# Kernel optimization log

Measured on AMD Instinct MI355X. Metric: run time of the kernel, lower is better.

The kernel has to match this reference:

```python
import jax, jax.numpy as jnp
import numpy as np

B, T, S = 16, 128, 128          # batch, temporal, spatial (road segments)
NIN, SIN = 3, 1                 # number / speed input feature sizes
NH, SH, DH = 64, 64, 128        # number-enc / speed-enc / decoder hidden
T_PREDICT = 20


def _p(k, shape, scale=0.05):
    return (jax.random.normal(k, shape) * scale).astype(jnp.float32)


def setup_inputs() -> dict:
    key = jax.random.key(0)
    ks = jax.random.split(key, 16)
    inp = {"input_data": jax.random.normal(ks[0], (B, T, S, NIN + SIN), dtype=jnp.float32)}
    # seg_model cells: LSTM gates driven by input x, own hidden h, spatial neighbors h_after/h_before
    inp.update(
        n_Wx=_p(ks[1], (NIN, 4 * NH)), n_Wh=_p(ks[2], (NH, 4 * NH)),
        n_Wa=_p(ks[3], (NH, 4 * NH)), n_Wb=_p(ks[4], (NH, 4 * NH)),
        n_b=jnp.zeros((4 * NH,), jnp.float32),
        s_Wx=_p(ks[5], (SIN, 4 * SH)), s_Wh=_p(ks[6], (SH, 4 * SH)),
        s_Wa=_p(ks[7], (SH, 4 * SH)), s_Wb=_p(ks[8], (SH, 4 * SH)),
        s_b=jnp.zeros((4 * SH,), jnp.float32),
        d_Wx=_p(ks[9], (NH + SH, 4 * DH)), d_Wh=_p(ks[10], (DH, 4 * DH)),
        d_Wa=_p(ks[11], (DH, 4 * DH)), d_Wb=_p(ks[12], (DH, 4 * DH)),
        d_b=jnp.zeros((4 * DH,), jnp.float32),
        on_W=_p(ks[13], (DH, 1)), on_b=jnp.zeros((1,), jnp.float32),
        os_W=_p(ks[14], (DH, 1)), os_b=jnp.zeros((1,), jnp.float32),
    )
    return inp


def _cell(x, h, c, ha, hb, Wx, Wh, Wa, Wb, b):
    g = x @ Wx + h @ Wh + ha @ Wa + hb @ Wb + b
    i, f, u, o = jnp.split(g, 4, axis=-1)
    c2 = jax.nn.sigmoid(f) * c + jax.nn.sigmoid(i) * jnp.tanh(u)
    return jax.nn.sigmoid(o) * jnp.tanh(c2), c2


def _shift(h):
    # h_after[s] = h[s+1], h_before[s] = h[s-1], zero-padded at the boundary
    z = jnp.zeros_like(h[:, :1])
    return jnp.concatenate([h[:, 1:], z], axis=1), jnp.concatenate([z, h[:, :-1]], axis=1)


def _next_input(former_number, next_x, output):
    # output: [B,S,2] = (number_out, speed_out)
    speed_in = next_x[:, :1, 3:]                                    # [B,1,1]
    speed_next = jnp.concatenate([speed_in, output[:, 1:, 1:]], axis=1)
    inflow = jnp.concatenate([next_x[:, 0:1, 1:2], output[:, :-1, 0:1]], axis=1)
    number_calc = former_number[:, :, 2:3] + inflow - output[:, :, 0:1]
    return jnp.concatenate([output[:, :, 0:1], inflow, number_calc, speed_next], axis=2)


def reference(input_data, n_Wx, n_Wh, n_Wa, n_Wb, n_b,
              s_Wx, s_Wh, s_Wa, s_Wb, s_b,
              d_Wx, d_Wh, d_Wa, d_Wb, d_b,
              on_W, on_b, os_W, os_b):
    b, t, s, _ = input_data.shape
    zeros = lambda hdim: jnp.zeros((b, s, hdim), input_data.dtype)
    init = (zeros(NH), zeros(NH), zeros(SH), zeros(SH), zeros(DH), zeros(DH))

    def step(carry, xs):
        hn, cn, hs, cs, hd, cd = carry
        x_t, x_tp1 = xs
        hn_a, hn_b = _shift(hn)
        hs_a, hs_b = _shift(hs)
        hd_a, hd_b = _shift(hd)
        num = x_t[:, :, :NIN]
        spd = x_t[:, :, NIN:]
        hn, cn = _cell(num, hn, cn, hn_a, hn_b, n_Wx, n_Wh, n_Wa, n_Wb, n_b)
        hs, cs = _cell(spd, hs, cs, hs_a, hs_b, s_Wx, s_Wh, s_Wa, s_Wb, s_b)
        dec_in = jnp.concatenate([hn, hs], axis=2)
        hd, cd = _cell(dec_in, hd, cd, hd_a, hd_b, d_Wx, d_Wh, d_Wa, d_Wb, d_b)
        output = jnp.concatenate([hd @ on_W + on_b, hd @ os_W + os_b], axis=2)
        data = _next_input(num, x_tp1, output)
        return (hn, cn, hs, cs, hd, cd), data

    xs = (jnp.moveaxis(input_data[:, :-1], 1, 0),   # x_t,   t = 0..T-2 (time-major)
          jnp.moveaxis(input_data[:, 1:], 1, 0))    # x_{t+1}
    _, datas = jax.lax.scan(step, init, xs)          # [T-1, B, S, 4]
    # original writes outputs only for time >= t_predict; slicing is equivalent
    return jnp.moveaxis(datas[T_PREDICT:], 0, 1)     # [B, T-T_PREDICT-1, S, 4]
```

## Files before the change

### kernel.cpp

```cpp
#include <hip/hip_runtime.h>

constexpr int B_ = 16, T_ = 128, S_ = 128;
constexpr int ROWS = B_ * S_;
constexpr int NSTEPS = T_ - 1;
constexpr int TPRED = 20;
constexpr int TOUT = NSTEPS - TPRED;
constexpr int TB = 512;
constexpr int NBLK = 256;

constexpr int OFF_HN = 0;
constexpr int OFF_HS = OFF_HN + 131072;
constexpr int OFF_HD = OFF_HS + 131072;
constexpr int OFF_CN = OFF_HD + 262144;
constexpr int OFF_CS = OFF_CN + 131072;
constexpr int OFF_CD = OFF_CS + 131072;
constexpr int OFF_OUTS = OFF_CD + 262144;
constexpr int ZERO_DW = OFF_OUTS + NSTEPS * ROWS * 2;
constexpr int OFF_NPK = ZERO_DW;
constexpr int NPK_DW = 16 * 7 * 256;
constexpr int OFF_SPK = OFF_NPK + NPK_DW;
constexpr int OFF_DPK = OFF_SPK + NPK_DW;
constexpr int DPK_DW = 32 * 16 * 256;
constexpr int PACK_DWORDS = 2 * NPK_DW + DPK_DW;

typedef _Float16 half8 __attribute__((ext_vector_type(8)));
typedef float float4v __attribute__((ext_vector_type(4)));

__device__ __forceinline__ float sigm(float x) { return 1.f / (1.f + __expf(-x)); }
__device__ __forceinline__ float tanh_(float x) { return 2.f / (1.f + __expf(-2.f * x)) - 1.f; }
__device__ __forceinline__ unsigned int pack2(float a, float b) {
    union { unsigned int u; _Float16 h[2]; } x;
    x.h[0] = (_Float16)a; x.h[1] = (_Float16)b; return x.u;
}

__global__ __launch_bounds__(256) void pack_weights(
    const float* __restrict__ nWx, const float* __restrict__ nWh,
    const float* __restrict__ nWa, const float* __restrict__ nWb, const float* __restrict__ nb,
    const float* __restrict__ sWx, const float* __restrict__ sWh,
    const float* __restrict__ sWa, const float* __restrict__ sWb, const float* __restrict__ sb,
    const float* __restrict__ dWx, const float* __restrict__ dWh,
    const float* __restrict__ dWa, const float* __restrict__ dWb,
    unsigned int* __restrict__ wsu)
{
    int idx = blockIdx.x * 256 + threadIdx.x;
    if (idx >= PACK_DWORDS) return;
    if (idx < 2 * NPK_DW) {
        bool isS = idx >= NPK_DW;
        int dn = isS ? idx - NPK_DW : idx;
        int tile = dn >> 8;
        int e = (dn & 255) * 2;
        int lane = e >> 3, j0 = e & 7;
        int quad = lane >> 4;
        int nt = tile / 7, tt = tile % 7;
        int col = nt * 16 + (lane & 15);
        float v0, v1;
        if (tt < 6) {
            const float* W = isS ? ((tt < 2) ? sWh : (tt < 4) ? sWa : sWb)
                                 : ((tt < 2) ? nWh : (tt < 4) ? nWa : nWb);
            int k = (tt & 1) * 32 + quad * 8 + j0;
            v0 = W[k * 256 + col]; v1 = W[(k + 1) * 256 + col];
        } else {
            int kl = quad * 8 + j0;
            auto xv = [&](int k) -> float {
                if (!isS) { if (k < 3) return nWx[k * 256 + col]; if (k == 3) return nb[col]; return 0.f; }
                else      { if (k == 4) return sWx[col]; if (k == 5) return sb[col]; return 0.f; }
            };
            v0 = xv(kl); v1 = xv(kl + 1);
        }
        wsu[(isS ? OFF_SPK : OFF_NPK) + dn] = pack2(v0, v1);
    } else {
        int dd = idx - 2 * NPK_DW;
        int tile = dd >> 8;
        int e = (dd & 255) * 2;
        int lane = e >> 3, j0 = e & 7;
        int quad = lane >> 4;
        int nt = tile >> 4, tt = tile & 15;
        const float* W = (tt < 4) ? dWx : (tt < 8) ? dWh : (tt < 12) ? dWa : dWb;
        int k = (tt & 3) * 32 + quad * 8 + j0;
        int col = nt * 16 + (lane & 15);
        wsu[OFF_DPK + dd] = pack2(W[k * 512 + col], W[(k + 1) * 512 + col]);
    }
}

__global__ __launch_bounds__(TB) void pipe_kernel(
    int li,
    const float* __restrict__ input,
    const float* __restrict__ db,
    const float* __restrict__ onW, const float* __restrict__ osW,
    float* __restrict__ ws)
{
    const int tid = threadIdx.x;
    const int wave = tid >> 6, lane = tid & 63;
    const int quad = lane >> 4, l15 = lane & 15;
    const int blk = blockIdx.x;

    _Float16* hnG = (_Float16*)((unsigned int*)ws + OFF_HN);
    _Float16* hsG = (_Float16*)((unsigned int*)ws + OFF_HS);
    _Float16* hdG = (_Float16*)((unsigned int*)ws + OFF_HD);
    float* outs = ws + OFF_OUTS;
    const _Float16* pd = (const _Float16*)((const unsigned int*)ws + OFF_DPK);

    __shared__ __align__(16) _Float16 sh_h[34 * 72];
    __shared__ __align__(16) _Float16 sh_xa[32 * 40];
    __shared__ __align__(16) _Float16 sh_hd[34 * 136];
    __shared__ __align__(16) _Float16 sh_dec[32 * 136];
    __shared__ float sh_hdnew[32 * 64];

    if (blk < 128) {
        if (li > 126) return;
        const int pr = blk >> 1, cell = blk & 1;
        const int r0 = pr * 32;
        const int b = r0 >> 7;
        const int s0 = r0 & 127;
        const bool leftOK = (pr & 3) != 0;
        const bool rightOK = (pr & 3) != 3;
        const int pin = (li + 1) & 1, pout = li & 1;
        const _Float16* hC = (cell ? hsG : hnG) + (size_t)pin * ROWS * 64;
        _Float16* hN = (cell ? hsG : hnG) + (size_t)pout * ROWS * 64;
        float* cB = ws + (cell ? OFF_CS : OFF_CN);

        for (int i = tid; i < 1088; i += TB) {
            int row = i >> 5, p = i & 31;
            int grow = r0 + row - 1;
            bool v = (row == 0) ? leftOK : ((row == 33) ? rightOK : true);
            unsigned int val = v ? ((const unsigned int*)hC)[(size_t)grow * 32 + p] : 0u;
            *(unsigned int*)(sh_h + row * 72 + 2 * p) = val;
        }
        for (int i = tid; i < 544; i += TB) {
            int r = i / 17, d = 3 + (i % 17);
            ((unsigned int*)sh_xa)[r * 20 + d] = 0u;
        }
        if (tid < 32) {
            const float* xp = input + ((size_t)(b * T_ + li) * S_ + (s0 + tid)) * 4;
            unsigned int* row = (unsigned int*)sh_xa + tid * 20;
            row[0] = pack2(xp[0], xp[1]);
            row[1] = pack2(xp[2], 1.f);
            row[2] = pack2(xp[3], 1.f);
        }
        __syncthreads();

        const int tl = wave >> 2, sub = wave & 3;
        const _Float16* pk = (const _Float16*)((const unsigned int*)ws + (cell ? OFF_SPK : OFF_NPK));
        const int rb = 1 + tl * 16 + l15;
        half8 ah0 = *(const half8*)(sh_h + rb * 72 + quad * 8);
        half8 ah1 = *(const half8*)(sh_h + rb * 72 + 32 + quad * 8);
        half8 aa0 = *(const half8*)(sh_h + (rb + 1) * 72 + quad * 8);
        half8 aa1 = *(const half8*)(sh_h + (rb + 1) * 72 + 32 + quad * 8);
        half8 ab0 = *(const half8*)(sh_h + (rb - 1) * 72 + quad * 8);
        half8 ab1 = *(const half8*)(sh_h + (rb - 1) * 72 + 32 + quad * 8);
        half8 ax  = *(const half8*)(sh_xa + (tl * 16 + l15) * 40 + quad * 8);
        float4v acc[4];
#pragma unroll
        for (int g = 0; g < 4; ++g) acc[g] = (float4v){0.f, 0.f, 0.f, 0.f};
#pragma unroll
        for (int g = 0; g < 4; ++g) {
            const _Float16* base = pk + (size_t)(4 * g + sub) * 7 * 512 + lane * 8;
            acc[g] = __builtin_amdgcn_mfma_f32_16x16x32_f16(ah0, *(const half8*)(base),        acc[g], 0, 0, 0);
            acc[g] = __builtin_amdgcn_mfma_f32_16x16x32_f16(ah1, *(const half8*)(base + 512),  acc[g], 0, 0, 0);
            acc[g] = __builtin_amdgcn_mfma_f32_16x16x32_f16(aa0, *(const half8*)(base + 1024), acc[g], 0, 0, 0);
            acc[g] = __builtin_amdgcn_mfma_f32_16x16x32_f16(aa1, *(const half8*)(base + 1536), acc[g], 0, 0, 0);
            acc[g] = __builtin_amdgcn_mfma_f32_16x16x32_f16(ab0, *(const half8*)(base + 2048), acc[g], 0, 0, 0);
            acc[g] = __builtin_amdgcn_mfma_f32_16x16x32_f16(ab1, *(const half8*)(base + 2560), acc[g], 0, 0, 0);
            acc[g] = __builtin_amdgcn_mfma_f32_16x16x32_f16(ax,  *(const half8*)(base + 3072), acc[g], 0, 0, 0);
        }
        size_t cIdx = ((size_t)((pr * 2 + tl) * 4 + sub) * 64 + lane) * 4;
        float4v cold = *(const float4v*)(cB + cIdx);
        float4v cnew;
        const int kcol = 16 * sub + l15;
#pragma unroll
        for (int r = 0; r < 4; ++r) {
            float c2 = sigm(acc[1][r]) * cold[r] + sigm(acc[0][r]) * tanh_(acc[2][r]);
            float h2 = sigm(acc[3][r]) * tanh_(c2);
            cnew[r] = c2;
            int row = tl * 16 + quad * 4 + r;
            hN[(size_t)(r0 + row) * 64 + kcol] = (_Float16)h2;
        }
        *(float4v*)(cB + cIdx) = cnew;
    } else {
        if (li < 1) return;
        const int bb = blk - 128;
        const int pr = bb >> 1, ch = bb & 1;
        const int t = li - 1;
        const int r0 = pr * 32;
        const bool leftOK = (pr & 3) != 0;
        const bool rightOK = (pr & 3) != 3;
        const int pinD = li & 1;
        const int poutD = (li - 1) & 1;
        const int pdec = (li - 1) & 1;
        const _Float16* hdC = hdG + (size_t)pinD * ROWS * 128;
        _Float16* hdN = hdG + (size_t)poutD * ROWS * 128;
        const _Float16* hnC = hnG + (size_t)pdec * ROWS * 64;
        const _Float16* hsC = hsG + (size_t)pdec * ROWS * 64;
        float* cd = ws + OFF_CD;

        for (int i = tid; i < 2176; i += TB) {
            int row = i >> 6, p = i & 63;
            int grow = r0 + row - 1;
            bool v = (row == 0) ? leftOK : ((row == 33) ? rightOK : true);
            unsigned int val = v ? ((const unsigned int*)hdC)[(size_t)grow * 64 + p] : 0u;
            *(unsigned int*)(sh_hd + row * 136 + 2 * p) = val;
        }
        for (int i = tid; i < 2048; i += TB) {
            bool isHs = i >= 1024;
            int j = isHs ? i - 1024 : i;
            int r = j >> 5, p = j & 31;
            const unsigned int* src = (const unsigned int*)(isHs ? hsC : hnC);
            *(unsigned int*)(sh_dec + r * 136 + (isHs ? 64 : 0) + 2 * p) = src[(size_t)(r0 + r) * 32 + p];
        }
        __syncthreads();

        const int tl = wave >> 2, sub = wave & 3;
        const int rb = 1 + tl * 16 + l15;
        const int rdec = tl * 16 + l15;
        half8 aD[4], aH[4], aA[4], aB4[4];
#pragma unroll
        for (int kt = 0; kt < 4; ++kt) {
            aD[kt]  = *(const half8*)(sh_dec + rdec * 136 + kt * 32 + quad * 8);
            aH[kt]  = *(const half8*)(sh_hd + rb * 136 + kt * 32 + quad * 8);
            aA[kt]  = *(const half8*)(sh_hd + (rb + 1) * 136 + kt * 32 + quad * 8);
            aB4[kt] = *(const half8*)(sh_hd + (rb - 1) * 136 + kt * 32 + quad * 8);
        }
        float4v acc[4];
#pragma unroll
        for (int g = 0; g < 4; ++g) acc[g] = (float4v){0.f, 0.f, 0.f, 0.f};
#pragma unroll
        for (int g = 0; g < 4; ++g) {
            const _Float16* base = pd + (size_t)(g * 8 + ch * 4 + sub) * 16 * 512 + lane * 8;
#pragma unroll
            for (int kt = 0; kt < 4; ++kt)
                acc[g] = __builtin_amdgcn_mfma_f32_16x16x32_f16(aD[kt],  *(const half8*)(base + kt * 512),        acc[g], 0, 0, 0);
#pragma unroll
            for (int kt = 0; kt < 4; ++kt)
                acc[g] = __builtin_amdgcn_mfma_f32_16x16x32_f16(aH[kt],  *(const half8*)(base + (4 + kt) * 512),  acc[g], 0, 0, 0);
#pragma unroll
            for (int kt = 0; kt < 4; ++kt)
                acc[g] = __builtin_amdgcn_mfma_f32_16x16x32_f16(aA[kt],  *(const half8*)(base + (8 + kt) * 512),  acc[g], 0, 0, 0);
#pragma unroll
            for (int kt = 0; kt < 4; ++kt)
                acc[g] = __builtin_amdgcn_mfma_f32_16x16x32_f16(aB4[kt], *(const half8*)(base + (12 + kt) * 512), acc[g], 0, 0, 0);
        }
        const int kd = ch * 64 + sub * 16 + l15;
        float bi = db[kd], bf = db[128 + kd], bu = db[256 + kd], bo = db[384 + kd];
        float* cPtr = cd + ((size_t)(((pr * 2 + ch) * 2 + tl) * 4 + sub) * 64 + lane) * 4;
        float4v cold = *(float4v*)cPtr, cnew;
#pragma unroll
        for (int r = 0; r < 4; ++r) {
            float c2 = sigm(acc[1][r] + bf) * cold[r] + sigm(acc[0][r] + bi) * tanh_(acc[2][r] + bu);
            float h2 = sigm(acc[3][r] + bo) * tanh_(c2);
            cnew[r] = c2;
            int row = tl * 16 + quad * 4 + r;
            hdN[(size_t)(r0 + row) * 128 + kd] = (_Float16)h2;
            sh_hdnew[row * 64 + sub * 16 + l15] = h2;
        }
        *(float4v*)cPtr = cnew;
        __syncthreads();

        {
            int p = tid >> 3, l8 = tid & 7;
            int row = p >> 1, head = p & 1;
            const float* W = (head ? osW : onW) + ch * 64;
            float partial = 0.f;
#pragma unroll
            for (int k = 0; k < 64; k += 8) partial += sh_hdnew[row * 64 + k + l8] * W[k + l8];
#pragma unroll
            for (int off = 4; off; off >>= 1) partial += __shfl_down(partial, off, 8);
            if (l8 == 0) atomicAdd(&outs[((size_t)t * ROWS + (r0 + row)) * 2 + head], partial);
        }
    }
}

__global__ __launch_bounds__(256) void assemble_kernel(
    const float* __restrict__ input, const float* __restrict__ ws,
    const float* __restrict__ onb, const float* __restrict__ osb,
    float* __restrict__ out)
{
    const float* outs = ws + OFF_OUTS;
    int idx = blockIdx.x * 256 + threadIdx.x;
    if (idx >= B_ * TOUT * S_) return;
    int s = idx & 127;
    int tmp = idx >> 7;
    int tt = tmp % TOUT;
    int b = tmp / TOUT;
    int t = tt + TPRED;
    int row = b * S_ + s;
    float ob0 = onb[0], ob1 = osb[0];
    float o0 = outs[((size_t)t * ROWS + row) * 2 + 0] + ob0;
    float o1 = outs[((size_t)t * ROWS + row) * 2 + 1] + ob1;
    float inflow = (s == 0) ? input[(((size_t)b * T_ + (t + 1)) * S_ + 0) * 4 + 1]
                            : (outs[((size_t)t * ROWS + row - 1) * 2 + 0] + ob0);
    float numc = input[(((size_t)b * T_ + t) * S_ + s) * 4 + 2] + inflow - o0;
    float spd = (s == 0) ? input[(((size_t)b * T_ + (t + 1)) * S_ + 0) * 4 + 3] : o1;
    float4 v = make_float4(o0, inflow, numc, spd);
    reinterpret_cast<float4*>(out)[idx] = v;
}

extern "C" void kernel_launch(void* const* d_in, const int* in_sizes, int n_in,
                              void* d_out, int out_size, void* d_ws, size_t ws_size,
                              hipStream_t stream) {
    const float* input = (const float*)d_in[0];
    const float* nWx = (const float*)d_in[1];
    const float* nWh = (const float*)d_in[2];
    const float* nWa = (const float*)d_in[3];
    const float* nWb = (const float*)d_in[4];
    const float* nb  = (const float*)d_in[5];
    const float* sWx = (const float*)d_in[6];
    const float* sWh = (const float*)d_in[7];
    const float* sWa = (const float*)d_in[8];
    const float* sWb = (const float*)d_in[9];
    const float* sb  = (const float*)d_in[10];
    const float* dWx = (const float*)d_in[11];
    const float* dWh = (const float*)d_in[12];
    const float* dWa = (const float*)d_in[13];
    const float* dWb = (const float*)d_in[14];
    const float* db  = (const float*)d_in[15];
    const float* onW = (const float*)d_in[16];
    const float* onb = (const float*)d_in[17];
    const float* osW = (const float*)d_in[18];
    const float* osb = (const float*)d_in[19];

    float* ws = (float*)d_ws;

    hipMemsetAsync(ws, 0, (size_t)ZERO_DW * 4, stream);

    pack_weights<<<dim3((PACK_DWORDS + 255) / 256), dim3(256), 0, stream>>>(
        nWx, nWh, nWa, nWb, nb, sWx, sWh, sWa, sWb, sb,
        dWx, dWh, dWa, dWb, (unsigned int*)ws);

    for (int li = 0; li <= NSTEPS; ++li) {
        pipe_kernel<<<dim3(NBLK), dim3(TB), 0, stream>>>(
            li, input, db, onW, osW, ws);
    }

    int nout = B_ * TOUT * S_;
    assemble_kernel<<<dim3((nout + 255) / 256), dim3(256), 0, stream>>>(
        input, ws, onb, osb, (float*)d_out);
}
```

Before: 1.410 ms.

## Move decoder input-projection GEMM into encoder blocks via fp32 partial buffer

The encoder blocks now also multiply their freshly computed hidden state by the decoder's input weights (d_Wx slice) and write fp32 gate partials to a new double-buffered workspace region. The decoder blocks no longer stage hn/hs into shared memory or run the 16 MFMAs for the input term. Instead they start their accumulators from the sum of the two partials. This moves work off the decoder's critical path and balances load between the two block groups, at the cost of extra global fp32 traffic, an added barrier in the encoder path, and changed ping-pong parity for hd.

```diff
diff --git a/kernel.cpp b/kernel.cpp
--- a/kernel.cpp
+++ b/kernel.cpp
@@ -14,7 +14,9 @@
 constexpr int OFF_CN = OFF_HD + 262144;
 constexpr int OFF_CS = OFF_CN + 131072;
 constexpr int OFF_CD = OFF_CS + 131072;
-constexpr int OFF_OUTS = OFF_CD + 262144;
+constexpr int OFF_GP = OFF_CD + 262144;
+constexpr int GP_DW = 2 * 64 * 2 * 8 * 4 * 2 * 256;
+constexpr int OFF_OUTS = OFF_GP + GP_DW;
 constexpr int ZERO_DW = OFF_OUTS + NSTEPS * ROWS * 2;
 constexpr int OFF_NPK = ZERO_DW;
 constexpr int NPK_DW = 16 * 7 * 256;
@@ -97,13 +99,14 @@
     _Float16* hnG = (_Float16*)((unsigned int*)ws + OFF_HN);
     _Float16* hsG = (_Float16*)((unsigned int*)ws + OFF_HS);
     _Float16* hdG = (_Float16*)((unsigned int*)ws + OFF_HD);
+    float* gpart = ws + OFF_GP;
     float* outs = ws + OFF_OUTS;
     const _Float16* pd = (const _Float16*)((const unsigned int*)ws + OFF_DPK);
 
     __shared__ __align__(16) _Float16 sh_h[34 * 72];
     __shared__ __align__(16) _Float16 sh_xa[32 * 40];
+    __shared__ __align__(16) _Float16 sh_dh[32 * 72];
     __shared__ __align__(16) _Float16 sh_hd[34 * 136];
-    __shared__ __align__(16) _Float16 sh_dec[32 * 136];
     __shared__ float sh_hdnew[32 * 64];
 
     if (blk < 128) {
@@ -140,42 +143,70 @@
         __syncthreads();
 
         const int tl = wave >> 2, sub = wave & 3;
-        const _Float16* pk = (const _Float16*)((const unsigned int*)ws + (cell ? OFF_SPK : OFF_NPK));
-        const int rb = 1 + tl * 16 + l15;
-        half8 ah0 = *(const half8*)(sh_h + rb * 72 + quad * 8);
-        half8 ah1 = *(const half8*)(sh_h + rb * 72 + 32 + quad * 8);
-        half8 aa0 = *(const half8*)(sh_h + (rb + 1) * 72 + quad * 8);
-        half8 aa1 = *(const half8*)(sh_h + (rb + 1) * 72 + 32 + quad * 8);
-        half8 ab0 = *(const half8*)(sh_h + (rb - 1) * 72 + quad * 8);
-        half8 ab1 = *(const half8*)(sh_h + (rb - 1) * 72 + 32 + quad * 8);
-        half8 ax  = *(const half8*)(sh_xa + (tl * 16 + l15) * 40 + quad * 8);
-        float4v acc[4];
-#pragma unroll
-        for (int g = 0; g < 4; ++g) acc[g] = (float4v){0.f, 0.f, 0.f, 0.f};
-#pragma unroll
-        for (int g = 0; g < 4; ++g) {
-            const _Float16* base = pk + (size_t)(4 * g + sub) * 7 * 512 + lane * 8;
-            acc[g] = __builtin_amdgcn_mfma_f32_16x16x32_f16(ah0, *(const half8*)(base),        acc[g], 0, 0, 0);
-            acc[g] = __builtin_amdgcn_mfma_f32_16x16x32_f16(ah1, *(const half8*)(base + 512),  acc[g], 0, 0, 0);
-            acc[g] = __builtin_amdgcn_mfma_f32_16x16x32_f16(aa0, *(const half8*)(base + 1024), acc[g], 0, 0, 0);
-            acc[g] = __builtin_amdgcn_mfma_f32_16x16x32_f16(aa1, *(const half8*)(base + 1536), acc[g], 0, 0, 0);
-            acc[g] = __builtin_amdgcn_mfma_f32_16x16x32_f16(ab0, *(const half8*)(base + 2048), acc[g], 0, 0, 0);
-            acc[g] = __builtin_amdgcn_mfma_f32_16x16x32_f16(ab1, *(const half8*)(base + 2560), acc[g], 0, 0, 0);
-            acc[g] = __builtin_amdgcn_mfma_f32_16x16x32_f16(ax,  *(const half8*)(base + 3072), acc[g], 0, 0, 0);
-        }
-        size_t cIdx = ((size_t)((pr * 2 + tl) * 4 + sub) * 64 + lane) * 4;
-        float4v cold = *(const float4v*)(cB + cIdx);
-        float4v cnew;
-        const int kcol = 16 * sub + l15;
-#pragma unroll
-        for (int r = 0; r < 4; ++r) {
-            float c2 = sigm(acc[1][r]) * cold[r] + sigm(acc[0][r]) * tanh_(acc[2][r]);
-            float h2 = sigm(acc[3][r]) * tanh_(c2);
-            cnew[r] = c2;
-            int row = tl * 16 + quad * 4 + r;
-            hN[(size_t)(r0 + row) * 64 + kcol] = (_Float16)h2;
-        }
-        *(float4v*)(cB + cIdx) = cnew;
+        {
+            const _Float16* pk = (const _Float16*)((const unsigned int*)ws + (cell ? OFF_SPK : OFF_NPK));
+            const int rb = 1 + tl * 16 + l15;
+            half8 ah0 = *(const half8*)(sh_h + rb * 72 + quad * 8);
+            half8 ah1 = *(const half8*)(sh_h + rb * 72 + 32 + quad * 8);
+            half8 aa0 = *(const half8*)(sh_h + (rb + 1) * 72 + quad * 8);
+            half8 aa1 = *(const half8*)(sh_h + (rb + 1) * 72 + 32 + quad * 8);
+            half8 ab0 = *(const half8*)(sh_h + (rb - 1) * 72 + quad * 8);
+            half8 ab1 = *(const half8*)(sh_h + (rb - 1) * 72 + 32 + quad * 8);
+            half8 ax  = *(const half8*)(sh_xa + (tl * 16 + l15) * 40 + quad * 8);
+            float4v acc[4];
+#pragma unroll
+            for (int g = 0; g < 4; ++g) acc[g] = (float4v){0.f, 0.f, 0.f, 0.f};
+#pragma unroll
+            for (int g = 0; g < 4; ++g) {
+                const _Float16* base = pk + (size_t)(4 * g + sub) * 7 * 512 + lane * 8;
+                acc[g] = __builtin_amdgcn_mfma_f32_16x16x32_f16(ah0, *(const half8*)(base),        acc[g], 0, 0, 0);
+                acc[g] = __builtin_amdgcn_mfma_f32_16x16x32_f16(ah1, *(const half8*)(base + 512),  acc[g], 0, 0, 0);
+                acc[g] = __builtin_amdgcn_mfma_f32_16x16x32_f16(aa0, *(const half8*)(base + 1024), acc[g], 0, 0, 0);
+                acc[g] = __builtin_amdgcn_mfma_f32_16x16x32_f16(aa1, *(const half8*)(base + 1536), acc[g], 0, 0, 0);
+                acc[g] = __builtin_amdgcn_mfma_f32_16x16x32_f16(ab0, *(const half8*)(base + 2048), acc[g], 0, 0, 0);
+                acc[g] = __builtin_amdgcn_mfma_f32_16x16x32_f16(ab1, *(const half8*)(base + 2560), acc[g], 0, 0, 0);
+                acc[g] = __builtin_amdgcn_mfma_f32_16x16x32_f16(ax,  *(const half8*)(base + 3072), acc[g], 0, 0, 0);
+            }
+            size_t cIdx = ((size_t)((pr * 2 + tl) * 4 + sub) * 64 + lane) * 4;
+            float4v cold = *(const float4v*)(cB + cIdx);
+            float4v cnew;
+            const int kcol = 16 * sub + l15;
+#pragma unroll
+            for (int r = 0; r < 4; ++r) {
+                float c2 = sigm(acc[1][r]) * cold[r] + sigm(acc[0][r]) * tanh_(acc[2][r]);
+                float h2 = sigm(acc[3][r]) * tanh_(c2);
+                cnew[r] = c2;
+                int row = tl * 16 + quad * 4 + r;
+                hN[(size_t)(r0 + row) * 64 + kcol] = (_Float16)h2;
+                sh_dh[row * 72 + kcol] = (_Float16)h2;
+            }
+            *(float4v*)(cB + cIdx) = cnew;
+        }
+        __syncthreads();
+
+        {
+            const int ct = wave;
+            half8 aD[2][2];
+#pragma unroll
+            for (int t2 = 0; t2 < 2; ++t2)
+#pragma unroll
+                for (int ktl = 0; ktl < 2; ++ktl)
+                    aD[t2][ktl] = *(const half8*)(sh_dh + (t2 * 16 + l15) * 72 + ktl * 32 + quad * 8);
+            float* gp = gpart + ((((size_t)(li & 1) * 64 + pr) * 2 + cell) * 8 + ct) * (4 * 2 * 256);
+#pragma unroll
+            for (int g = 0; g < 4; ++g) {
+                const _Float16* base = pd + ((size_t)(g * 8 + ct) * 16 + 2 * cell) * 512 + lane * 8;
+                half8 b0 = *(const half8*)(base);
+                half8 b1 = *(const half8*)(base + 512);
+#pragma unroll
+                for (int t2 = 0; t2 < 2; ++t2) {
+                    float4v acc = (float4v){0.f, 0.f, 0.f, 0.f};
+                    acc = __builtin_amdgcn_mfma_f32_16x16x32_f16(aD[t2][0], b0, acc, 0, 0, 0);
+                    acc = __builtin_amdgcn_mfma_f32_16x16x32_f16(aD[t2][1], b1, acc, 0, 0, 0);
+                    *(float4v*)&gp[(g * 2 + t2) * 256 + lane * 4] = acc;
+                }
+            }
+        }
     } else {
         if (li < 1) return;
         const int bb = blk - 128;
@@ -185,12 +216,9 @@
         const bool leftOK = (pr & 3) != 0;
         const bool rightOK = (pr & 3) != 3;
         const int pinD = li & 1;
-        const int poutD = (li - 1) & 1;
-        const int pdec = (li - 1) & 1;
+        const int poutD = (li + 1) & 1;
         const _Float16* hdC = hdG + (size_t)pinD * ROWS * 128;
         _Float16* hdN = hdG + (size_t)poutD * ROWS * 128;
-        const _Float16* hnC = hnG + (size_t)pdec * ROWS * 64;
-        const _Float16* hsC = hsG + (size_t)pdec * ROWS * 64;
         float* cd = ws + OFF_CD;
 
         for (int i = tid; i < 2176; i += TB) {
@@ -200,35 +228,29 @@
             unsigned int val = v ? ((const unsigned int*)hdC)[(size_t)grow * 64 + p] : 0u;
             *(unsigned int*)(sh_hd + row * 136 + 2 * p) = val;
         }
-        for (int i = tid; i < 2048; i += TB) {
-            bool isHs = i >= 1024;
-            int j = isHs ? i - 1024 : i;
-            int r = j >> 5, p = j & 31;
-            const unsigned int* src = (const unsigned int*)(isHs ? hsC : hnC);
-            *(unsigned int*)(sh_dec + r * 136 + (isHs ? 64 : 0) + 2 * p) = src[(size_t)(r0 + r) * 32 + p];
-        }
         __syncthreads();
 
         const int tl = wave >> 2, sub = wave & 3;
+        const int ct2 = ch * 4 + sub;
+        const int par = (li + 1) & 1;
+        const float* gp0 = gpart + ((((size_t)par * 64 + pr) * 2 + 0) * 8 + ct2) * (4 * 2 * 256);
+        const float* gp1 = gpart + ((((size_t)par * 64 + pr) * 2 + 1) * 8 + ct2) * (4 * 2 * 256);
+        float4v acc[4];
+#pragma unroll
+        for (int g = 0; g < 4; ++g)
+            acc[g] = *(const float4v*)&gp0[(g * 2 + tl) * 256 + lane * 4]
+                   + *(const float4v*)&gp1[(g * 2 + tl) * 256 + lane * 4];
         const int rb = 1 + tl * 16 + l15;
-        const int rdec = tl * 16 + l15;
-        half8 aD[4], aH[4], aA[4], aB4[4];
+        half8 aH[4], aA[4], aB4[4];
 #pragma unroll
         for (int kt = 0; kt < 4; ++kt) {
-            aD[kt]  = *(const half8*)(sh_dec + rdec * 136 + kt * 32 + quad * 8);
             aH[kt]  = *(const half8*)(sh_hd + rb * 136 + kt * 32 + quad * 8);
             aA[kt]  = *(const half8*)(sh_hd + (rb + 1) * 136 + kt * 32 + quad * 8);
             aB4[kt] = *(const half8*)(sh_hd + (rb - 1) * 136 + kt * 32 + quad * 8);
         }
-        float4v acc[4];
-#pragma unroll
-        for (int g = 0; g < 4; ++g) acc[g] = (float4v){0.f, 0.f, 0.f, 0.f};
 #pragma unroll
         for (int g = 0; g < 4; ++g) {
-            const _Float16* base = pd + (size_t)(g * 8 + ch * 4 + sub) * 16 * 512 + lane * 8;
-#pragma unroll
-            for (int kt = 0; kt < 4; ++kt)
-                acc[g] = __builtin_amdgcn_mfma_f32_16x16x32_f16(aD[kt],  *(const half8*)(base + kt * 512),        acc[g], 0, 0, 0);
+            const _Float16* base = pd + (size_t)(g * 8 + ct2) * 16 * 512 + lane * 8;
 #pragma unroll
             for (int kt = 0; kt < 4; ++kt)
                 acc[g] = __builtin_amdgcn_mfma_f32_16x16x32_f16(aH[kt],  *(const half8*)(base + (4 + kt) * 512),  acc[g], 0, 0, 0);
@@ -239,7 +261,7 @@
             for (int kt = 0; kt < 4; ++kt)
                 acc[g] = __builtin_amdgcn_mfma_f32_16x16x32_f16(aB4[kt], *(const half8*)(base + (12 + kt) * 512), acc[g], 0, 0, 0);
         }
-        const int kd = ch * 64 + sub * 16 + l15;
+        const int kd = ct2 * 16 + l15;
         float bi = db[kd], bf = db[128 + kd], bu = db[256 + kd], bo = db[384 + kd];
         float* cPtr = cd + ((size_t)(((pr * 2 + ch) * 2 + tl) * 4 + sub) * 64 + lane) * 4;
         float4v cold = *(float4v*)cPtr, cnew;
```

Result: slower. 1.515 ms (+7.5%).
